# Kernel optimization log

Hardware: AMD Instinct MI355X
Metric: run time of the kernel (lower is better)

The kernel has to match this reference:

```python
import jax, jax.numpy as jnp
import numpy as np

MARGIN = 0.3
NUM_CLASSES = 32  # includes label 0, which the mask logic treats specially


def setup_inputs() -> dict:
    key = jax.random.key(0)
    k1, k2 = jax.random.split(key)
    n, d = 4096, 2048
    inputs = jax.random.normal(k1, (n, d), dtype=jnp.float32)
    targets = jax.random.randint(k2, (n,), 0, NUM_CLASSES, dtype=jnp.int64)
    return {"inputs": inputs, "targets": targets}


def reference(inputs, targets):
    # Pairwise euclidean distance matrix [n, n]
    sq = jnp.sum(inputs * inputs, axis=1)  # [n]
    dist2 = sq[:, None] + sq[None, :] - 2.0 * (inputs @ inputs.T)
    dist = jnp.sqrt(jnp.maximum(dist2, 1e-12))

    # Mask semantics from the torch code:
    #   mask == 1  : same label (hard-positive pool; includes diagonal)
    #   mask == 0  : different labels AND at least one of the pair has label 0
    #   mask == -1 : different labels, both nonzero (excluded from mining)
    ti, tj = targets[:, None], targets[None, :]
    same = ti == tj
    zero_neg = (~same) & ((ti == 0) | (tj == 0))

    neg_inf = jnp.asarray(-jnp.inf, dist.dtype)
    pos_inf = jnp.asarray(jnp.inf, dist.dtype)
    dist_ap = jnp.max(jnp.where(same, dist, neg_inf), axis=1)      # hardest positive per row
    row_min = jnp.min(jnp.where(zero_neg, dist, pos_inf), axis=1)  # hardest label-0 negative

    # Torch code checks row 0 only (mask[0]) for the presence of mask==0 entries;
    # if row 0 has none, ALL dist_an are set to 0. Reproduce faithfully.
    row0_has_zero = jnp.any(zero_neg[0])
    dist_an = jnp.where(row0_has_zero, row_min, jnp.zeros_like(row_min))

    # MarginRankingLoss with y = 1: mean(relu(-(dist_an - dist_ap) + margin))
    loss = jnp.mean(jax.nn.relu(dist_ap - dist_an + MARGIN))
    return loss
```

## Files before the change

kernel.cpp:

```cpp
#include <hip/hip_runtime.h>
#include <hip/hip_bf16.h>
#include <math.h>

#define N 4096
#define K 2048
#define NC 32
#define MARGIN 0.3f

#define BK 128
#define NITER (K / BK)
#define DIAG_BLOCKS 288
#define CROSS_BLOCKS 192
#define GRID (DIAG_BLOCKS + CROSS_BLOCKS)

typedef float f32x4 __attribute__((ext_vector_type(4)));
typedef __bf16 bf16x8 __attribute__((ext_vector_type(8)));

__device__ __forceinline__ void glds16(const void* g, void* l) {
  __builtin_amdgcn_global_load_lds(
      (const __attribute__((address_space(1))) void*)g,
      (__attribute__((address_space(3))) void*)l, 16, 0, 0);
}

__device__ __forceinline__ int imin(int a, int b) { return a < b ? a : b; }

__global__ __launch_bounds__(256) void hist_kernel(
    const int* __restrict__ tg, int* __restrict__ cnt, int* __restrict__ off,
    int* __restrict__ cursor, int* __restrict__ flag, int* __restrict__ done) {
  __shared__ int h[NC];
  int t = threadIdx.x;
  if (t < NC) h[t] = 0;
  __syncthreads();
  const int4* tg4 = (const int4*)tg;
  for (int i = t; i < N / 4; i += 256) {
    int4 v = tg4[i];
    atomicAdd(&h[v.x], 1); atomicAdd(&h[v.y], 1);
    atomicAdd(&h[v.z], 1); atomicAdd(&h[v.w], 1);
  }
  __syncthreads();
  if (t == 0) {
    int acc = 0;
    for (int c = 0; c < NC; c++) {
      cnt[c] = h[c];
      off[c] = acc;
      cursor[c] = acc;
      acc += h[c];
    }
    int t0 = tg[0];
    flag[0] = (t0 == 0) ? (N - h[0] > 0) : (h[0] > 0);
    done[0] = 0;
  }
}

__global__ __launch_bounds__(256) void convert_kernel(
    const float* __restrict__ X, const int* __restrict__ tg,
    __bf16* __restrict__ Xg, float* __restrict__ sqg,
    unsigned int* __restrict__ ap, unsigned int* __restrict__ an,
    int* __restrict__ cursor) {
  int row = blockIdx.x;
  int t = threadIdx.x;
  const float* xr = X + (size_t)row * K;

  float4 v0 = ((const float4*)xr)[t * 2 + 0];
  float4 v1 = ((const float4*)xr)[t * 2 + 1];

  float s = v0.x * v0.x + v0.y * v0.y + v0.z * v0.z + v0.w * v0.w +
            v1.x * v1.x + v1.y * v1.y + v1.z * v1.z + v1.w * v1.w;

  bf16x8 b;
  b[0] = (__bf16)v0.x; b[1] = (__bf16)v0.y; b[2] = (__bf16)v0.z; b[3] = (__bf16)v0.w;
  b[4] = (__bf16)v1.x; b[5] = (__bf16)v1.y; b[6] = (__bf16)v1.z; b[7] = (__bf16)v1.w;

  #pragma unroll
  for (int m = 32; m; m >>= 1) s += __shfl_xor(s, m);

  __shared__ float wred[4];
  __shared__ int spos;
  if ((t & 63) == 0) wred[t >> 6] = s;
  if (t == 0) spos = atomicAdd(&cursor[tg[row]], 1);
  __syncthreads();
  int pos = spos;

  ((bf16x8*)(Xg + (size_t)pos * K))[t] = b;
  if (t == 0) {
    sqg[pos] = wred[0] + wred[1] + wred[2] + wred[3];
    ap[pos] = 0u;
    an[pos] = 0x7f800000u;
  }
}

__global__ __launch_bounds__(256) void gemm_reduce_kernel(
    const __bf16* __restrict__ Xg, const float* __restrict__ sqg,
    const int* __restrict__ cnt, const int* __restrict__ off,
    unsigned int* __restrict__ ap, unsigned int* __restrict__ an,
    const int* __restrict__ flag, int* __restrict__ done,
    float* __restrict__ out) {
  __shared__ __align__(16) __bf16 sA[2][64 * BK];
  __shared__ __align__(16) __bf16 sB[2][64 * BK];
  __shared__ int s_islast;
  __shared__ float wred[4];

  int b = blockIdx.x;
  int t = threadIdx.x;

  bool active = true, diag = true;
  int i0g = 0, iend = 1, j0g = 0, jend = 1;
  if (b < DIAG_BLOCKS) {
    int c = b / 9, sub = b % 9;
    int sti = sub / 3, stj = sub % 3;
    int o = off[c], n = cnt[c];
    if (n == 0 || sti * 64 >= n || stj * 64 >= n) active = false;
    i0g = o + sti * 64; iend = o + n;
    j0g = o + stj * 64; jend = o + n;
  } else {
    int idx = b - DIAG_BLOCKS;
    int it = idx >> 6, jt = idx & 63;
    int n0 = cnt[0];
    int j0 = n0 + jt * 64;
    if (n0 == 0 || it * 64 >= n0 || j0 >= N) active = false;
    i0g = it * 64; iend = n0;
    j0g = j0; jend = N;
    diag = false;
  }

  if (active) {
    int w = t >> 6, l = t & 63;
    int wi = w >> 1, wj = w & 1;
    int quad = l >> 4, lr = l & 15;

    const char* gA[4]; const char* gB[4];
    int rr = t >> 4, cbl = t & 15;
    int cbg = cbl ^ rr;
    #pragma unroll
    for (int r = 0; r < 4; r++) {
      int row_l = r * 16 + rr;
      int ra = imin(i0g + row_l, iend - 1);
      int rb = imin(j0g + row_l, jend - 1);
      gA[r] = (const char*)(Xg + (size_t)ra * K) + cbg * 16;
      gB[r] = (const char*)(Xg + (size_t)rb * K) + cbg * 16;
    }

    int aoff[2][4], boff[2][4];
    #pragma unroll
    for (int ti = 0; ti < 2; ti++)
      #pragma unroll
      for (int kc = 0; kc < 4; kc++) {
        int cb = kc * 4 + quad;
        int sw = (cb ^ lr) * 16;
        aoff[ti][kc] = (wi * 32 + ti * 16 + lr) * 256 + sw;
        boff[ti][kc] = (wj * 32 + ti * 16 + lr) * 256 + sw;
      }

    f32x4 acc[2][2];
    acc[0][0] = (f32x4)0.f; acc[0][1] = (f32x4)0.f;
    acc[1][0] = (f32x4)0.f; acc[1][1] = (f32x4)0.f;

    auto stage = [&](int buf, int itk) {
      int koff = itk * (BK * 2);
      char* la = (char*)sA + buf * 16384 + t * 16;
      char* lb = (char*)sB + buf * 16384 + t * 16;
      #pragma unroll
      for (int r = 0; r < 4; r++) {
        glds16(gA[r] + koff, la + r * 4096);
        glds16(gB[r] + koff, lb + r * 4096);
      }
    };

    auto compute = [&](int buf) {
      const char* bufA = (const char*)sA + buf * 16384;
      const char* bufB = (const char*)sB + buf * 16384;
      #pragma unroll
      for (int kc = 0; kc < 4; kc++) {
        bf16x8 a0 = *(const bf16x8*)(bufA + aoff[0][kc]);
        bf16x8 a1 = *(const bf16x8*)(bufA + aoff[1][kc]);
        bf16x8 b0 = *(const bf16x8*)(bufB + boff[0][kc]);
        bf16x8 b1 = *(const bf16x8*)(bufB + boff[1][kc]);
        acc[0][0] = __builtin_amdgcn_mfma_f32_16x16x32_bf16(a0, b0, acc[0][0], 0, 0, 0);
        acc[0][1] = __builtin_amdgcn_mfma_f32_16x16x32_bf16(a0, b1, acc[0][1], 0, 0, 0);
        acc[1][0] = __builtin_amdgcn_mfma_f32_16x16x32_bf16(a1, b0, acc[1][0], 0, 0, 0);
        acc[1][1] = __builtin_amdgcn_mfma_f32_16x16x32_bf16(a1, b1, acc[1][1], 0, 0, 0);
      }
    };

    stage(0, 0);
    for (int itk = 0; itk < NITER - 1; ++itk) {
      int cur = itk & 1;
      __builtin_amdgcn_s_barrier();
      stage(cur ^ 1, itk + 1);
      __builtin_amdgcn_s_waitcnt(0x0F78);
      __builtin_amdgcn_s_barrier();
      __builtin_amdgcn_sched_barrier(0);
      compute(cur);
    }
    __builtin_amdgcn_s_barrier();
    __builtin_amdgcn_s_waitcnt(0x0F70);
    __builtin_amdgcn_s_barrier();
    __builtin_amdgcn_sched_barrier(0);
    compute((NITER - 1) & 1);

    int jgc[2]; float sqj[2];
    #pragma unroll
    for (int tj = 0; tj < 2; tj++) {
      int jg = j0g + wj * 32 + tj * 16 + lr;
      jgc[tj] = imin(jg, jend - 1);
      sqj[tj] = sqg[jgc[tj]];
    }

    if (diag) {
      #pragma unroll
      for (int ti = 0; ti < 2; ti++) {
        #pragma unroll
        for (int r = 0; r < 4; r++) {
          int ig = i0g + wi * 32 + ti * 16 + quad * 4 + r;
          int igc = imin(ig, iend - 1);
          float sqi = sqg[igc];
          float apm = 0.f;
          #pragma unroll
          for (int tj = 0; tj < 2; tj++) {
            float d2 = sqi + sqj[tj] - 2.f * acc[ti][tj][r];
            apm = fmaxf(apm, sqrtf(fmaxf(d2, 1e-12f)));
          }
          #pragma unroll
          for (int m = 1; m < 16; m <<= 1) apm = fmaxf(apm, __shfl_xor(apm, m));
          if (lr == 0) atomicMax(ap + igc, __float_as_uint(apm));
        }
      }
    } else {
      float colmin[2] = {INFINITY, INFINITY};
      #pragma unroll
      for (int ti = 0; ti < 2; ti++) {
        #pragma unroll
        for (int r = 0; r < 4; r++) {
          int ig = i0g + wi * 32 + ti * 16 + quad * 4 + r;
          int igc = imin(ig, iend - 1);
          float sqi = sqg[igc];
          float anm = INFINITY;
          #pragma unroll
          for (int tj = 0; tj < 2; tj++) {
            float d2 = sqi + sqj[tj] - 2.f * acc[ti][tj][r];
            float d = sqrtf(fmaxf(d2, 1e-12f));
            anm = fminf(anm, d);
            colmin[tj] = fminf(colmin[tj], d);
          }
          #pragma unroll
          for (int m = 1; m < 16; m <<= 1) anm = fminf(anm, __shfl_xor(anm, m));
          if (lr == 0) atomicMin(an + igc, __float_as_uint(anm));
        }
      }
      #pragma unroll
      for (int tj = 0; tj < 2; tj++) {
        float v = colmin[tj];
        v = fminf(v, __shfl_xor(v, 16));
        v = fminf(v, __shfl_xor(v, 32));
        if (quad == 0) atomicMin(an + jgc[tj], __float_as_uint(v));
      }
    }
  }

  __syncthreads();
  if (t == 0) {
    __threadfence();
    int ticket = __hip_atomic_fetch_add(done, 1, __ATOMIC_ACQ_REL,
                                        __HIP_MEMORY_SCOPE_AGENT);
    s_islast = (ticket == GRID - 1);
  }
  __syncthreads();
  if (s_islast) {
    int has = flag[0];
    float s = 0.f;
    for (int i = t; i < N; i += 256) {
      unsigned int au = __hip_atomic_load(ap + i, __ATOMIC_RELAXED,
                                          __HIP_MEMORY_SCOPE_AGENT);
      unsigned int nu = __hip_atomic_load(an + i, __ATOMIC_RELAXED,
                                          __HIP_MEMORY_SCOPE_AGENT);
      float a = __uint_as_float(au);
      float bb = has ? __uint_as_float(nu) : 0.f;
      s += fmaxf(a - bb + MARGIN, 0.f);
    }
    #pragma unroll
    for (int m = 32; m; m >>= 1) s += __shfl_xor(s, m);
    if ((t & 63) == 0) wred[t >> 6] = s;
    __syncthreads();
    if (t == 0) out[0] = (wred[0] + wred[1] + wred[2] + wred[3]) / (float)N;
  }
}

extern "C" void kernel_launch(void* const* d_in, const int* in_sizes, int n_in,
                              void* d_out, int out_size, void* d_ws,
                              size_t ws_size, hipStream_t stream) {
  const float* X = (const float*)d_in[0];
  const int* tg = (const int*)d_in[1];
  float* out = (float*)d_out;

  char* ws = (char*)d_ws;
  __bf16* Xg = (__bf16*)ws;
  size_t o = (size_t)N * K * 2;
  float* sqg = (float*)(ws + o); o += (size_t)N * 4;
  unsigned int* ap = (unsigned int*)(ws + o); o += (size_t)N * 4;
  unsigned int* an = (unsigned int*)(ws + o); o += (size_t)N * 4;
  int* cnt = (int*)(ws + o); o += NC * 4;
  int* off = (int*)(ws + o); o += NC * 4;
  int* cur = (int*)(ws + o); o += NC * 4;
  int* flag = (int*)(ws + o); o += 4;
  int* done = (int*)(ws + o); o += 4;

  hist_kernel<<<1, 256, 0, stream>>>(tg, cnt, off, cur, flag, done);
  convert_kernel<<<N, 256, 0, stream>>>(X, tg, Xg, sqg, ap, an, cur);
  gemm_reduce_kernel<<<GRID, 256, 0, stream>>>(Xg, sqg, cnt, off, ap, an,
                                               flag, done, out);
}
```

Baseline: 141.4 us.

## Exploit symmetry in per-class diagonal tiles and convert four rows per block

The same-class distance tiles are now computed only for the upper triangle: 6 tiles per class instead of 9. Off-diagonal tiles also reduce a column maximum and apply it with atomicMax to the transposed rows, which removes redundant GEMM work. Separately, the convert kernel now maps one wavefront per row, four rows per block, and uses a wave shuffle in place of the shared-memory reduction and block barrier. The symmetric path adds extra column reductions and atomics per tile.

New measurement: 139.6 us. Within noise of the previous version (-1.2%).

```diff
diff --git a/kernel.cpp b/kernel.cpp
--- a/kernel.cpp
+++ b/kernel.cpp
@@ -9,7 +9,7 @@
 
 #define BK 128
 #define NITER (K / BK)
-#define DIAG_BLOCKS 288
+#define DIAG_BLOCKS 192
 #define CROSS_BLOCKS 192
 #define GRID (DIAG_BLOCKS + CROSS_BLOCKS)
 
@@ -57,33 +57,45 @@
     __bf16* __restrict__ Xg, float* __restrict__ sqg,
     unsigned int* __restrict__ ap, unsigned int* __restrict__ an,
     int* __restrict__ cursor) {
-  int row = blockIdx.x;
   int t = threadIdx.x;
-  const float* xr = X + (size_t)row * K;
-
-  float4 v0 = ((const float4*)xr)[t * 2 + 0];
-  float4 v1 = ((const float4*)xr)[t * 2 + 1];
-
-  float s = v0.x * v0.x + v0.y * v0.y + v0.z * v0.z + v0.w * v0.w +
-            v1.x * v1.x + v1.y * v1.y + v1.z * v1.z + v1.w * v1.w;
-
-  bf16x8 b;
-  b[0] = (__bf16)v0.x; b[1] = (__bf16)v0.y; b[2] = (__bf16)v0.z; b[3] = (__bf16)v0.w;
-  b[4] = (__bf16)v1.x; b[5] = (__bf16)v1.y; b[6] = (__bf16)v1.z; b[7] = (__bf16)v1.w;
+  int row = blockIdx.x * 4 + (t >> 6);
+  int lane = t & 63;
+  const float4* xr = (const float4*)(X + (size_t)row * K);
+
+  float4 v[8];
+  #pragma unroll
+  for (int q = 0; q < 4; q++) {
+    int chunk = q * 64 + lane;
+    v[2 * q]     = xr[chunk * 2];
+    v[2 * q + 1] = xr[chunk * 2 + 1];
+  }
+
+  float s = 0.f;
+  bf16x8 b[4];
+  #pragma unroll
+  for (int q = 0; q < 4; q++) {
+    float4 a0 = v[2 * q], a1 = v[2 * q + 1];
+    s += a0.x * a0.x + a0.y * a0.y + a0.z * a0.z + a0.w * a0.w +
+         a1.x * a1.x + a1.y * a1.y + a1.z * a1.z + a1.w * a1.w;
+    b[q][0] = (__bf16)a0.x; b[q][1] = (__bf16)a0.y;
+    b[q][2] = (__bf16)a0.z; b[q][3] = (__bf16)a0.w;
+    b[q][4] = (__bf16)a1.x; b[q][5] = (__bf16)a1.y;
+    b[q][6] = (__bf16)a1.z; b[q][7] = (__bf16)a1.w;
+  }
 
   #pragma unroll
   for (int m = 32; m; m >>= 1) s += __shfl_xor(s, m);
 
-  __shared__ float wred[4];
-  __shared__ int spos;
-  if ((t & 63) == 0) wred[t >> 6] = s;
-  if (t == 0) spos = atomicAdd(&cursor[tg[row]], 1);
-  __syncthreads();
-  int pos = spos;
-
-  ((bf16x8*)(Xg + (size_t)pos * K))[t] = b;
-  if (t == 0) {
-    sqg[pos] = wred[0] + wred[1] + wred[2] + wred[3];
+  int pos = 0;
+  if (lane == 0) pos = atomicAdd(&cursor[tg[row]], 1);
+  pos = __shfl(pos, 0);
+
+  bf16x8* dst = (bf16x8*)(Xg + (size_t)pos * K);
+  #pragma unroll
+  for (int q = 0; q < 4; q++) dst[q * 64 + lane] = b[q];
+
+  if (lane == 0) {
+    sqg[pos] = s;
     ap[pos] = 0u;
     an[pos] = 0x7f800000u;
   }
@@ -103,15 +115,17 @@
   int b = blockIdx.x;
   int t = threadIdx.x;
 
-  bool active = true, diag = true;
+  bool active = true, diag = true, dcol = false;
   int i0g = 0, iend = 1, j0g = 0, jend = 1;
   if (b < DIAG_BLOCKS) {
-    int c = b / 9, sub = b % 9;
-    int sti = sub / 3, stj = sub % 3;
+    int c = b / 6, p = b % 6;
+    int sti = (p < 3) ? 0 : (p < 5 ? 1 : 2);
+    int stj = (p < 3) ? p : (p < 5 ? p - 2 : 2);
     int o = off[c], n = cnt[c];
     if (n == 0 || sti * 64 >= n || stj * 64 >= n) active = false;
     i0g = o + sti * 64; iend = o + n;
     j0g = o + stj * 64; jend = o + n;
+    dcol = (sti != stj);
   } else {
     int idx = b - DIAG_BLOCKS;
     int it = idx >> 6, jt = idx & 63;
@@ -207,6 +221,7 @@
     }
 
     if (diag) {
+      float colmax[2] = {0.f, 0.f};
       #pragma unroll
       for (int ti = 0; ti < 2; ti++) {
         #pragma unroll
@@ -218,11 +233,22 @@
           #pragma unroll
           for (int tj = 0; tj < 2; tj++) {
             float d2 = sqi + sqj[tj] - 2.f * acc[ti][tj][r];
-            apm = fmaxf(apm, sqrtf(fmaxf(d2, 1e-12f)));
+            float d = sqrtf(fmaxf(d2, 1e-12f));
+            apm = fmaxf(apm, d);
+            colmax[tj] = fmaxf(colmax[tj], d);
           }
           #pragma unroll
           for (int m = 1; m < 16; m <<= 1) apm = fmaxf(apm, __shfl_xor(apm, m));
           if (lr == 0) atomicMax(ap + igc, __float_as_uint(apm));
+        }
+      }
+      if (dcol) {
+        #pragma unroll
+        for (int tj = 0; tj < 2; tj++) {
+          float v = colmax[tj];
+          v = fmaxf(v, __shfl_xor(v, 16));
+          v = fmaxf(v, __shfl_xor(v, 32));
+          if (quad == 0) atomicMax(ap + jgc[tj], __float_as_uint(v));
         }
       }
     } else {
@@ -305,7 +331,7 @@
   int* done = (int*)(ws + o); o += 4;
 
   hist_kernel<<<1, 256, 0, stream>>>(tg, cnt, off, cur, flag, done);
-  convert_kernel<<<N, 256, 0, stream>>>(X, tg, Xg, sqg, ap, an, cur);
+  convert_kernel<<<N / 4, 256, 0, stream>>>(X, tg, Xg, sqg, ap, an, cur);
   gemm_reduce_kernel<<<GRID, 256, 0, stream>>>(Xg, sqg, cnt, off, ap, an,
                                                flag, done, out);
 }
```
